# Optimization experiments

Hardware: AMD Instinct MI355X
Metric: run time of the kernel (lower is better)

The kernel has to match this reference:

```python
import jax, jax.numpy as jnp
import numpy as np

ALPHA = 10.0
DELTA = 0.0005
N = 16777216  # array_length


def setup_inputs() -> dict:
    key = jax.random.key(0)
    k1, k2 = jax.random.split(key)
    # learned parameter: in the original module this is initialized to linspace(0,1,N);
    # we use uniform [0,1] so the piecewise-linear search path is non-degenerate.
    indices = jax.random.uniform(k1, (N,), dtype=jnp.float32)
    array = jax.random.normal(k2, (N,), dtype=jnp.float32)
    return {"indices": indices, "array": array}


def reference(indices, array):
    # clamp learned knot positions to [0, 1]
    clamped = jnp.clip(indices, 0.0, 1.0)
    # piecewise-linear function f with x-knots = clamped, y-values = array.
    # jnp.interp requires ascending knots, so sort (x, y) pairs by x.
    order = jnp.argsort(clamped)
    xs = clamped[order]
    ys = array[order]
    # vectorized version of the per-index loop:
    #   left_item = f(clamped[i-1] + delta), this_item = f(clamped[i] - delta)
    q_left = clamped[:-1] + DELTA   # [N-1]
    q_this = clamped[1:] - DELTA    # [N-1]
    f_left = jnp.interp(q_left, xs, ys)
    f_this = jnp.interp(q_this, xs, ys)
    gap = jnp.maximum(f_left - f_this, 0.0)
    return ALPHA * jnp.sum(gap)
```

## Files before the change

### kernel.cpp

```cpp
#include <hip/hip_runtime.h>
#include <stdint.h>

#define ALPHA_C 10.0f
#define DELTA_C 0.0005f

typedef unsigned long long u64;
typedef unsigned u32;
typedef unsigned short u16;

#define KB2   (1u << 22)
#define NREG  8192
#define FPR   512
#define CAP   4096
#define Q38MAX ((1ULL << 38) - 1)

#define OLDKB (1u << 22)
#define SCAN_BLOCKS 1024
#define SCAN_TPB 256
#define SCAN_PER_THREAD 16

__device__ __forceinline__ float clamp01(float x) {
    return fminf(fmaxf(x, 0.0f), 1.0f);
}
__device__ __forceinline__ u64 q38_of(float x) {
    double d = (double)clamp01(x) * 274877906944.0;
    u64 q = (u64)d;
    return q > Q38MAX ? Q38MAX : q;
}
__device__ __forceinline__ u16 f2bf(float f) {
    u32 b = __float_as_uint(f);
    return (u16)((b + 0x8000u) >> 16);
}
__device__ __forceinline__ float bf2f(u32 h) {
    return __uint_as_float(h << 16);
}


__global__ void __launch_bounds__(256) k_hist(const float* __restrict__ ind,
                                              u32* __restrict__ cnt8k, int n) {
    __shared__ u32 lh[NREG];
    for (int k = threadIdx.x; k < (int)NREG; k += 256) lh[k] = 0;
    __syncthreads();
    int stride = gridDim.x * blockDim.x;
    for (int i = blockIdx.x * blockDim.x + threadIdx.x; i < n; i += stride)
        atomicAdd(&lh[(u32)(q38_of(ind[i]) >> 25)], 1u);
    __syncthreads();
    for (int k = threadIdx.x; k < (int)NREG; k += 256) {
        u32 v = lh[k];
        if (v) atomicAdd(&cnt8k[k], v);
    }
}

__global__ void __launch_bounds__(1024) k_scan8k(u32* __restrict__ cnt8k) {
    __shared__ u32 lds[1024];
    int tid = threadIdx.x;
    int base = tid * 8;
    u32 v[8]; u32 tot = 0;
#pragma unroll
    for (int k = 0; k < 8; ++k) { v[k] = cnt8k[base + k]; tot += v[k]; }
    lds[tid] = tot;
    __syncthreads();
    u32 x = tot;
    for (int s = 1; s < 1024; s <<= 1) {
        u32 y = (tid >= s) ? lds[tid - s] : 0u;
        __syncthreads();
        x += y; lds[tid] = x;
        __syncthreads();
    }
    u32 run = x - tot;
#pragma unroll
    for (int k = 0; k < 8; ++k) { u32 c = v[k]; cnt8k[base + k] = run; run += c; }
}

__global__ void k_coarse(const float* __restrict__ ind, const float* __restrict__ arr,
                         u32* __restrict__ cnt8k,
                         u32* __restrict__ recx, u64* __restrict__ reciy, int n) {
    int i = blockIdx.x * blockDim.x + threadIdx.x;
    if (i < n) {
        float x = ind[i];
        u32 r = (u32)(q38_of(x) >> 25);
        u32 e = atomicAdd(&cnt8k[r], 1u);
        recx[e] = __float_as_uint(x);
        reciy[e] = ((u64)(u32)i << 16) | (u64)f2bf(arr[i]);
    }
}

__global__ void __launch_bounds__(512) k_fine(const u32* __restrict__ cnt8k,
                                              u16* __restrict__ foff16,
                                              const u32* __restrict__ recx,
                                              u64* __restrict__ reciy_fdata) {
    __shared__ u32 sx[CAP];
    __shared__ u64 siy[CAP];
    __shared__ u32 incl[FPR];
    __shared__ u32 lexcl[FPR];
    __shared__ u32 lcnt[FPR];
    int r = blockIdx.x;
    u32 s = (r == 0) ? 0u : cnt8k[r - 1];
    u32 e = cnt8k[r];
    u32 cnt = e - s; if (cnt > CAP) cnt = CAP;
    for (u32 j = threadIdx.x; j < cnt; j += 512) { sx[j] = recx[s + j]; siy[j] = reciy_fdata[s + j]; }
    incl[threadIdx.x] = 0;
    lcnt[threadIdx.x] = 0;
    __syncthreads();
    for (u32 j = threadIdx.x; j < cnt; j += 512) {
        u32 lb = (u32)((q38_of(__uint_as_float(sx[j])) >> 16) & (FPR - 1));
        atomicAdd(&incl[lb], 1u);
    }
    __syncthreads();
    u32 myc = incl[threadIdx.x];
    u32 x = myc;
    for (int st = 1; st < FPR; st <<= 1) {
        u32 y = (threadIdx.x >= (u32)st) ? incl[threadIdx.x - st] : 0u;
        __syncthreads();
        x += y; incl[threadIdx.x] = x;
        __syncthreads();
    }
    lexcl[threadIdx.x] = x - myc;
    foff16[r * FPR + threadIdx.x] = (u16)x;
    __syncthreads();
    for (u32 j = threadIdx.x; j < cnt; j += 512) {
        u64 q = q38_of(__uint_as_float(sx[j]));
        u32 lb = (u32)((q >> 16) & (FPR - 1));
        u32 p = s + lexcl[lb] + atomicAdd(&lcnt[lb], 1u);
        u64 iy = siy[j];
        reciy_fdata[p] = ((q & 0xFFFFULL) << 40) | ((iy & 0xFFFFULL) << 24) | (iy >> 16);
    }
}

__device__ __forceinline__ void bucket_range(u32 b, const u32* __restrict__ cnt8k,
                                             const u16* __restrict__ foff16,
                                             u32* s, u32* e) {
    u32 r = b >> 9;
    u32 rbase = r ? cnt8k[r - 1] : 0u;
    u32 lb = b & (FPR - 1);
    *s = rbase + (lb ? (u32)foff16[b - 1] : 0u);
    *e = rbase + (u32)foff16[b];
}

__device__ float feval_q(u64 qq, const u32* __restrict__ cnt8k,
                         const u16* __restrict__ foff16, const u64* __restrict__ fdata) {
    u32 qb = (u32)(qq >> 16);
    u32 ql = (u32)(qq & 0xFFFFu);
    u32 s, e;
    bucket_range(qb, cnt8k, foff16, &s, &e);
    long long loK = -1;
    u64 hiK = ~0ULL;
    float loY = 0.0f, hiY = 0.0f;
    for (u32 p = s; p < e; ++p) {
        u64 d = fdata[p];
        u32 xlo = (u32)(d >> 40);
        u64 key = ((((u64)qb << 16) | xlo) << 24) | (d & 0xFFFFFFULL);
        float y = bf2f((u32)(d >> 24) & 0xFFFFu);
        if (xlo <= ql) { if ((long long)key >= loK) { loK = (long long)key; loY = y; } }
        else           { if (key < hiK)             { hiK = key;            hiY = y; } }
    }
    if (loK < 0) {
        u32 bl = qb;
        while (bl > 0) {
            --bl;
            u32 s2, e2;
            bucket_range(bl, cnt8k, foff16, &s2, &e2);
            if (e2 > s2) {
                for (u32 p = s2; p < e2; ++p) {
                    u64 d = fdata[p];
                    u64 key = ((((u64)bl << 16) | (d >> 40)) << 24) | (d & 0xFFFFFFULL);
                    if ((long long)key >= loK) { loK = (long long)key; loY = bf2f((u32)(d >> 24) & 0xFFFFu); }
                }
                break;
            }
        }
    }
    if (hiK == ~0ULL) {
        u32 br = qb;
        while (br < KB2 - 1) {
            ++br;
            u32 s2, e2;
            bucket_range(br, cnt8k, foff16, &s2, &e2);
            if (e2 > s2) {
                for (u32 p = s2; p < e2; ++p) {
                    u64 d = fdata[p];
                    u64 key = ((((u64)br << 16) | (d >> 40)) << 24) | (d & 0xFFFFFFULL);
                    if (key < hiK) { hiK = key; hiY = bf2f((u32)(d >> 24) & 0xFFFFu); }
                }
                break;
            }
        }
    }
    if (loK < 0) return hiY;
    if (hiK == ~0ULL) return loY;
    u64 loQ = (u64)loK >> 24;
    u64 hiQ = hiK >> 24;
    if (hiQ == loQ) return loY;
    float dq = (float)(qq - loQ);
    float dd = (float)(hiQ - loQ);
    return loY + (dq / dd) * (hiY - loY);
}

__global__ void __launch_bounds__(512) k_eval(const u32* __restrict__ cnt8k,
        const u16* __restrict__ foff16, const u64* __restrict__ fdata,
        u32* __restrict__ oval) {
    __shared__ u32 fend[FPR];
    int r = blockIdx.x;
    u32 s = r ? cnt8k[r - 1] : 0u;
    u32 e = cnt8k[r];
    fend[threadIdx.x] = s + (u32)foff16[r * FPR + threadIdx.x];
    __syncthreads();
    for (u32 t = s + threadIdx.x; t < e; t += 512) {
        u64 d = fdata[t];
        u32 lo = 0;
#pragma unroll
        for (u32 st = 256; st; st >>= 1) if (t >= fend[lo + st - 1]) lo += st;
        u64 xq = (((u64)((u32)r * FPR + lo)) << 16) | (d >> 40);
        u32 i = (u32)(d & 0xFFFFFFu);
        float x = (float)((double)xq * 3.63797880709171295e-12);
        float qpf = x + DELTA_C;
        float qmf = x - DELTA_C;
        u64 qp = q38_of(qpf);
        u64 qm = q38_of(qmf);
        float fp = feval_q(qp, cnt8k, foff16, fdata);
        float fm = feval_q(qm, cnt8k, foff16, fdata);
        oval[i] = ((u32)f2bf(fp) << 16) | (u32)f2bf(fm);
    }
}

__global__ void __launch_bounds__(256) k_pair2(const u32* __restrict__ oval,
                                               float* __restrict__ out, int n) {
    int stride = gridDim.x * blockDim.x;
    float sum = 0.0f;
    for (int j = blockIdx.x * blockDim.x + threadIdx.x; j < n - 1; j += stride) {
        u32 a = oval[j], b = oval[j + 1];
        sum += fmaxf(bf2f(a >> 16) - bf2f(b & 0xFFFFu), 0.0f);
    }
    float w = sum;
    for (int s = 32; s > 0; s >>= 1) w += __shfl_down(w, s, 64);
    __shared__ float wsum[4];
    if ((threadIdx.x & 63) == 0) wsum[threadIdx.x >> 6] = w;
    __syncthreads();
    if (threadIdx.x == 0)
        atomicAdd(out, ALPHA_C * (wsum[0] + wsum[1] + wsum[2] + wsum[3]));
}


__device__ __forceinline__ int bucket_of(float x) {
    int b = (int)(x * (float)OLDKB);
    b = b < 0 ? 0 : b;
    b = b > (int)OLDKB - 1 ? (int)OLDKB - 1 : b;
    return b;
}

__global__ void scan1(u32* __restrict__ off, u32* __restrict__ bsums) {
    __shared__ u32 lds[SCAN_TPB];
    int base = blockIdx.x * (SCAN_TPB * SCAN_PER_THREAD) + threadIdx.x * SCAN_PER_THREAD;
    u32 v[SCAN_PER_THREAD];
    u32 tot = 0;
#pragma unroll
    for (int k = 0; k < SCAN_PER_THREAD; ++k) { v[k] = off[base + k]; tot += v[k]; }
    lds[threadIdx.x] = tot;
    __syncthreads();
    u32 x = tot;
    for (int s = 1; s < SCAN_TPB; s <<= 1) {
        u32 y = (threadIdx.x >= (u32)s) ? lds[threadIdx.x - s] : 0u;
        __syncthreads();
        x += y; lds[threadIdx.x] = x;
        __syncthreads();
    }
    if (threadIdx.x == SCAN_TPB - 1) bsums[blockIdx.x] = x;
    u32 run = x - tot;
#pragma unroll
    for (int k = 0; k < SCAN_PER_THREAD; ++k) { u32 c = v[k]; off[base + k] = run; run += c; }
}

__global__ void scan2(u32* __restrict__ bsums) {
    __shared__ u32 lds[SCAN_BLOCKS];
    int tid = threadIdx.x;
    u32 v = bsums[tid];
    lds[tid] = v;
    __syncthreads();
    u32 x = v;
    for (int s = 1; s < SCAN_BLOCKS; s <<= 1) {
        u32 y = (tid >= s) ? lds[tid - s] : 0u;
        __syncthreads();
        x += y; lds[tid] = x;
        __syncthreads();
    }
    bsums[tid] = x - v;
}

__global__ void scan3(u32* __restrict__ off, const u32* __restrict__ bsums) {
    int base = blockIdx.x * (SCAN_TPB * SCAN_PER_THREAD);
    u32 add = bsums[blockIdx.x];
#pragma unroll
    for (int k = 0; k < SCAN_PER_THREAD; ++k)
        off[base + k * SCAN_TPB + threadIdx.x] += add;
}

__global__ void hist_kernel(const float* __restrict__ ind, u32* __restrict__ off, int n) {
    int i = blockIdx.x * blockDim.x + threadIdx.x;
    if (i < n) atomicAdd(&off[bucket_of(clamp01(ind[i]))], 1u);
}

__global__ void scatter_kernel(const float* __restrict__ ind, const float* __restrict__ arr,
                               u32* __restrict__ off, float2* __restrict__ buck, int n) {
    int i = blockIdx.x * blockDim.x + threadIdx.x;
    if (i < n) {
        float x = clamp01(ind[i]);
        u32 p = atomicAdd(&off[bucket_of(x)], 1u);
        buck[p] = make_float2(x, arr[i]);
    }
}

__device__ float feval(float q, const u32* __restrict__ off, const float2* __restrict__ buck) {
    int b = bucket_of(q);
    u32 s = (b == 0) ? 0u : off[b - 1];
    u32 e = off[b];
    float loX = -1e30f, loY = 0.0f, hiX = 1e30f, hiY = 0.0f;
    for (u32 u = s; u < e; ++u) {
        float2 p = buck[u];
        if (p.x <= q) { if (p.x >= loX) { loX = p.x; loY = p.y; } }
        else          { if (p.x <  hiX) { hiX = p.x; hiY = p.y; } }
    }
    if (loX == -1e30f) {
        int bl = b;
        while (bl > 0) {
            --bl;
            u32 s2 = (bl == 0) ? 0u : off[bl - 1];
            u32 e2 = off[bl];
            if (e2 > s2) {
                for (u32 u = s2; u < e2; ++u) {
                    float2 p = buck[u];
                    if (p.x >= loX) { loX = p.x; loY = p.y; }
                }
                break;
            }
        }
    }
    if (hiX == 1e30f) {
        int br = b;
        while (br < (int)OLDKB - 1) {
            ++br;
            u32 s2 = off[br - 1];
            u32 e2 = off[br];
            if (e2 > s2) {
                for (u32 u = s2; u < e2; ++u) {
                    float2 p = buck[u];
                    if (p.x < hiX) { hiX = p.x; hiY = p.y; }
                }
                break;
            }
        }
    }
    if (loX == -1e30f) return hiY;
    if (hiX ==  1e30f) return loY;
    return loY + (q - loX) * (hiY - loY) / (hiX - loX);
}

__global__ void query_kernel(const float* __restrict__ ind, const u32* __restrict__ off,
                             const float2* __restrict__ buck, float* __restrict__ out, int nterm) {
    int j = blockIdx.x * blockDim.x + threadIdx.x;
    float term = 0.0f;
    if (j < nterm) {
        float c0 = clamp01(ind[j]);
        float c1 = clamp01(ind[j + 1]);
        float fa = feval(c0 + DELTA_C, off, buck);
        float fb = feval(c1 - DELTA_C, off, buck);
        term = fmaxf(fa - fb, 0.0f);
    }
    float w = term;
    for (int s = 32; s > 0; s >>= 1) w += __shfl_down(w, s, 64);
    __shared__ float wsum[4];
    if ((threadIdx.x & 63) == 0) wsum[threadIdx.x >> 6] = w;
    __syncthreads();
    if (threadIdx.x == 0) atomicAdd(out, ALPHA_C * (wsum[0] + wsum[1] + wsum[2] + wsum[3]));
}


extern "C" void kernel_launch(void* const* d_in, const int* in_sizes, int n_in,
                              void* d_out, int out_size, void* d_ws, size_t ws_size,
                              hipStream_t stream) {
    const float* ind = (const float*)d_in[0];
    const float* arr = (const float*)d_in[1];
    float* out = (float*)d_out;
    int n = in_sizes[0];

    const int tpb = 256;
    int nblk = (n + tpb - 1) / tpb;
    uint8_t* w = (uint8_t*)d_ws;

    const size_t FOFF_SZ = (size_t)KB2 * 2;
    const size_t AUX = (size_t)1 << 20;
    size_t SZ8 = (size_t)n * 8, SZ4 = (size_t)n * 4;
    size_t base = FOFF_SZ + AUX;
    size_t need = base + SZ8 + SZ4;

    if (n <= (1 << 24) && ws_size >= need) {
        u16* foff16 = (u16*)w;
        u32* cnt8k  = (u32*)(w + FOFF_SZ);
        u64* reciy  = (u64*)(w + base);
        u32* recx   = (u32*)(w + base + SZ8);
        u32* oval   = (u32*)recx;

        hipMemsetAsync(cnt8k, 0, NREG * 4, stream);
        hipMemsetAsync(out, 0, sizeof(float) * (size_t)out_size, stream);

        k_hist<<<512, 256, 0, stream>>>(ind, cnt8k, n);
        k_scan8k<<<1, 1024, 0, stream>>>(cnt8k);
        k_coarse<<<nblk, tpb, 0, stream>>>(ind, arr, cnt8k, recx, reciy, n);
        k_fine<<<NREG, 512, 0, stream>>>(cnt8k, foff16, recx, reciy);
        k_eval<<<NREG, 512, 0, stream>>>(cnt8k, foff16, reciy, oval);
        k_pair2<<<2048, 256, 0, stream>>>(oval, out, n);
    } else {
        const size_t FO = (size_t)OLDKB * 4;
        u32* off = (u32*)w;
        u32* bsums = (u32*)(w + FO);
        float2* buck = (float2*)(w + FO + 4096);

        hipMemsetAsync(off, 0, FO, stream);
        hipMemsetAsync(out, 0, sizeof(float) * (size_t)out_size, stream);

        hist_kernel<<<nblk, tpb, 0, stream>>>(ind, off, n);
        scan1<<<SCAN_BLOCKS, SCAN_TPB, 0, stream>>>(off, bsums);
        scan2<<<1, SCAN_BLOCKS, 0, stream>>>(bsums);
        scan3<<<SCAN_BLOCKS, SCAN_TPB, 0, stream>>>(off, bsums);
        scatter_kernel<<<nblk, tpb, 0, stream>>>(ind, arr, off, buck, n);
        int nterm = n - 1;
        query_kernel<<<(nterm + tpb - 1) / tpb, tpb, 0, stream>>>(ind, off, buck, out, nterm);
    }
}
```

Before: 1.610 ms.

## Replace per-element coarse scatter with block-aggregated bucket scatter and fused fine sort

Replaces the coarse scatter, which did one global atomic per element, with a chunked kernel. Each block builds a shared-memory histogram over 4096 buckets, reserves ranges with one global atomic per bucket, then scatters packed 64-bit records. The fine sort now handles two coarse regions per block, reads the array values there rather than in the coarse pass, and writes the final packed records in place. cnt8k semantics shift from inclusive to exclusive offsets, which costs an extra prep kernel and a capacity limit (CAPB) that can truncate crowded buckets.

```diff
diff --git a/kernel.cpp b/kernel.cpp
--- a/kernel.cpp
+++ b/kernel.cpp
@@ -11,7 +11,11 @@
 #define KB2   (1u << 22)
 #define NREG  8192
 #define FPR   512
-#define CAP   4096
+#define NBK   4096
+#define RPB   2
+#define FPB   1024
+#define CAPB  4800
+#define ACHUNK 32768
 #define Q38MAX ((1ULL << 38) - 1)
 
 #define OLDKB (1u << 22)
@@ -72,58 +76,95 @@
     for (int k = 0; k < 8; ++k) { u32 c = v[k]; cnt8k[base + k] = run; run += c; }
 }
 
-__global__ void k_coarse(const float* __restrict__ ind, const float* __restrict__ arr,
-                         u32* __restrict__ cnt8k,
-                         u32* __restrict__ recx, u64* __restrict__ reciy, int n) {
-    int i = blockIdx.x * blockDim.x + threadIdx.x;
-    if (i < n) {
-        float x = ind[i];
-        u32 r = (u32)(q38_of(x) >> 25);
-        u32 e = atomicAdd(&cnt8k[r], 1u);
-        recx[e] = __float_as_uint(x);
-        reciy[e] = ((u64)(u32)i << 16) | (u64)f2bf(arr[i]);
-    }
-}
-
-__global__ void __launch_bounds__(512) k_fine(const u32* __restrict__ cnt8k,
-                                              u16* __restrict__ foff16,
-                                              const u32* __restrict__ recx,
-                                              u64* __restrict__ reciy_fdata) {
-    __shared__ u32 sx[CAP];
-    __shared__ u64 siy[CAP];
-    __shared__ u32 incl[FPR];
-    __shared__ u32 lexcl[FPR];
-    __shared__ u32 lcnt[FPR];
-    int r = blockIdx.x;
-    u32 s = (r == 0) ? 0u : cnt8k[r - 1];
-    u32 e = cnt8k[r];
-    u32 cnt = e - s; if (cnt > CAP) cnt = CAP;
-    for (u32 j = threadIdx.x; j < cnt; j += 512) { sx[j] = recx[s + j]; siy[j] = reciy_fdata[s + j]; }
-    incl[threadIdx.x] = 0;
-    lcnt[threadIdx.x] = 0;
-    __syncthreads();
-    for (u32 j = threadIdx.x; j < cnt; j += 512) {
-        u32 lb = (u32)((q38_of(__uint_as_float(sx[j])) >> 16) & (FPR - 1));
-        atomicAdd(&incl[lb], 1u);
-    }
-    __syncthreads();
-    u32 myc = incl[threadIdx.x];
-    u32 x = myc;
-    for (int st = 1; st < FPR; st <<= 1) {
-        u32 y = (threadIdx.x >= (u32)st) ? incl[threadIdx.x - st] : 0u;
-        __syncthreads();
-        x += y; incl[threadIdx.x] = x;
-        __syncthreads();
-    }
-    lexcl[threadIdx.x] = x - myc;
-    foff16[r * FPR + threadIdx.x] = (u16)x;
-    __syncthreads();
-    for (u32 j = threadIdx.x; j < cnt; j += 512) {
-        u64 q = q38_of(__uint_as_float(sx[j]));
-        u32 lb = (u32)((q >> 16) & (FPR - 1));
-        u32 p = s + lexcl[lb] + atomicAdd(&lcnt[lb], 1u);
-        u64 iy = siy[j];
-        reciy_fdata[p] = ((q & 0xFFFFULL) << 40) | ((iy & 0xFFFFULL) << 24) | (iy >> 16);
+__global__ void k_prep(const u32* __restrict__ cnt8k, u32* __restrict__ bcur) {
+    int b = blockIdx.x * 256 + threadIdx.x;
+    if (b < (int)NBK) bcur[b] = cnt8k[b * RPB];
+}
+
+__global__ void __launch_bounds__(256) k_bucket(const float* __restrict__ ind,
+                                                u32* __restrict__ bcur,
+                                                u64* __restrict__ rec, int n) {
+    __shared__ u32 hist[NBK];
+    __shared__ u32 base[NBK];
+    int cbase = blockIdx.x * ACHUNK;
+    for (u32 k = threadIdx.x; k < (u32)NBK; k += 256) hist[k] = 0;
+    __syncthreads();
+    for (int k = threadIdx.x; k < ACHUNK; k += 256) {
+        int i = cbase + k;
+        if (i >= n) break;
+        u32 bk = (u32)(q38_of(ind[i]) >> 26);
+        atomicAdd(&hist[bk], 1u);
+    }
+    __syncthreads();
+    for (u32 k = threadIdx.x; k < (u32)NBK; k += 256) {
+        u32 h = hist[k];
+        base[k] = h ? atomicAdd(&bcur[k], h) : 0u;
+    }
+    __syncthreads();
+    for (int k = threadIdx.x; k < ACHUNK; k += 256) {
+        int i = cbase + k;
+        if (i >= n) break;
+        u64 q = q38_of(ind[i]);
+        u32 bk = (u32)(q >> 26);
+        u32 d = atomicAdd(&base[bk], 1u);
+        rec[d] = (q << 24) | (u64)(u32)i;
+    }
+}
+
+__global__ void __launch_bounds__(256) k_group_fine(const u32* __restrict__ cnt8k,
+                                                    const float* __restrict__ arr,
+                                                    u16* __restrict__ foff16,
+                                                    u64* __restrict__ rec, int n) {
+    __shared__ u64 srec[CAPB];
+    __shared__ u32 sc[FPB];
+    __shared__ u32 lad[256];
+    int b = blockIdx.x;
+    u32 S = cnt8k[b * RPB];
+    u32 E = (b * RPB + RPB < (int)NREG) ? cnt8k[b * RPB + RPB] : (u32)n;
+    u32 cnt = E - S; if (cnt > CAPB) cnt = CAPB;
+    for (u32 j = threadIdx.x; j < cnt; j += 256) srec[j] = rec[S + j];
+    for (u32 f = threadIdx.x; f < (u32)FPB; f += 256) sc[f] = 0;
+    __syncthreads();
+    for (u32 j = threadIdx.x; j < cnt; j += 256) {
+        u32 fb = (u32)(srec[j] >> 40) & (FPB - 1);
+        atomicAdd(&sc[fb], 1u);
+    }
+    __syncthreads();
+    u32 c0 = sc[threadIdx.x * 4 + 0], c1 = sc[threadIdx.x * 4 + 1];
+    u32 c2 = sc[threadIdx.x * 4 + 2], c3 = sc[threadIdx.x * 4 + 3];
+    u32 tsum = c0 + c1 + c2 + c3;
+    lad[threadIdx.x] = tsum;
+    __syncthreads();
+    u32 x = tsum;
+    for (int st = 1; st < 256; st <<= 1) {
+        u32 y = (threadIdx.x >= (u32)st) ? lad[threadIdx.x - st] : 0u;
+        __syncthreads();
+        x += y; lad[threadIdx.x] = x;
+        __syncthreads();
+    }
+    u32 ex = x - tsum;
+    u32 e0 = ex, e1 = ex + c0, e2 = ex + c0 + c1, e3 = ex + c0 + c1 + c2;
+    sc[threadIdx.x * 4 + 0] = e0; sc[threadIdx.x * 4 + 1] = e1;
+    sc[threadIdx.x * 4 + 2] = e2; sc[threadIdx.x * 4 + 3] = e3;
+    __syncthreads();
+    {
+        u32 fb0 = threadIdx.x * 4;
+        u32 rs0 = sc[fb0 & ~511u];
+        u32 gb  = (u32)b * FPB + fb0;
+        foff16[gb + 0] = (u16)(e0 + c0 - rs0);
+        foff16[gb + 1] = (u16)(e1 + c1 - rs0);
+        foff16[gb + 2] = (u16)(e2 + c2 - rs0);
+        foff16[gb + 3] = (u16)(e3 + c3 - rs0);
+    }
+    __syncthreads();
+    for (u32 j = threadIdx.x; j < cnt; j += 256) {
+        u64 v = srec[j];
+        u32 fb  = (u32)(v >> 40) & (FPB - 1);
+        u32 i   = (u32)(v & 0xFFFFFFu);
+        u32 xlo = (u32)(v >> 24) & 0xFFFFu;
+        u32 ybf = f2bf(arr[i]);
+        u32 pos = atomicAdd(&sc[fb], 1u);
+        rec[S + pos] = ((u64)xlo << 40) | ((u64)ybf << 24) | (u64)i;
     }
 }
 
@@ -131,7 +172,7 @@
                                              const u16* __restrict__ foff16,
                                              u32* s, u32* e) {
     u32 r = b >> 9;
-    u32 rbase = r ? cnt8k[r - 1] : 0u;
+    u32 rbase = cnt8k[r];
     u32 lb = b & (FPR - 1);
     *s = rbase + (lb ? (u32)foff16[b - 1] : 0u);
     *e = rbase + (u32)foff16[b];
@@ -198,11 +239,11 @@
 
 __global__ void __launch_bounds__(512) k_eval(const u32* __restrict__ cnt8k,
         const u16* __restrict__ foff16, const u64* __restrict__ fdata,
-        u32* __restrict__ oval) {
+        u32* __restrict__ oval, int n) {
     __shared__ u32 fend[FPR];
     int r = blockIdx.x;
-    u32 s = r ? cnt8k[r - 1] : 0u;
-    u32 e = cnt8k[r];
+    u32 s = cnt8k[r];
+    u32 e = (r + 1 < (int)NREG) ? cnt8k[r + 1] : (u32)n;
     fend[threadIdx.x] = s + (u32)foff16[r * FPR + threadIdx.x];
     __syncthreads();
     for (u32 t = s + threadIdx.x; t < e; t += 512) {
@@ -395,18 +436,20 @@
     if (n <= (1 << 24) && ws_size >= need) {
         u16* foff16 = (u16*)w;
         u32* cnt8k  = (u32*)(w + FOFF_SZ);
-        u64* reciy  = (u64*)(w + base);
-        u32* recx   = (u32*)(w + base + SZ8);
-        u32* oval   = (u32*)recx;
+        u32* bcur   = (u32*)(w + FOFF_SZ + 32768);
+        u64* rec    = (u64*)(w + base);
+        u32* oval   = (u32*)(w + base + SZ8);
 
         hipMemsetAsync(cnt8k, 0, NREG * 4, stream);
         hipMemsetAsync(out, 0, sizeof(float) * (size_t)out_size, stream);
 
+        int abks = (n + ACHUNK - 1) / ACHUNK;
         k_hist<<<512, 256, 0, stream>>>(ind, cnt8k, n);
         k_scan8k<<<1, 1024, 0, stream>>>(cnt8k);
-        k_coarse<<<nblk, tpb, 0, stream>>>(ind, arr, cnt8k, recx, reciy, n);
-        k_fine<<<NREG, 512, 0, stream>>>(cnt8k, foff16, recx, reciy);
-        k_eval<<<NREG, 512, 0, stream>>>(cnt8k, foff16, reciy, oval);
+        k_prep<<<(NBK + 255) / 256, 256, 0, stream>>>(cnt8k, bcur);
+        k_bucket<<<abks, 256, 0, stream>>>(ind, bcur, rec, n);
+        k_group_fine<<<NBK, 256, 0, stream>>>(cnt8k, arr, foff16, rec, n);
+        k_eval<<<NREG, 512, 0, stream>>>(cnt8k, foff16, rec, oval, n);
         k_pair2<<<2048, 256, 0, stream>>>(oval, out, n);
     } else {
         const size_t FO = (size_t)OLDKB * 4;
```

After: 1.774 ms. 1.1x slower.

## Replace per-element global atomic scatter with block-local histogram and bulk reservation

Applied to the files above, without the earlier changes.

The coarse bucketing pass no longer does one global atomicAdd per element. Each block of 256 threads handles a 65536-element chunk: it builds a shared-memory histogram of bucket ids, reserves space per bucket with a single global atomic, then scatters using shared atomics. A separate cursor array copied from the scanned offsets keeps the end-offset semantics that later kernels expect. This cuts global atomic contention, but it reads the inputs twice, reduces parallelism to only 256 blocks, and uses 32KB of LDS per block.

```diff
diff --git a/kernel.cpp b/kernel.cpp
--- a/kernel.cpp
+++ b/kernel.cpp
@@ -12,6 +12,7 @@
 #define NREG  8192
 #define FPR   512
 #define CAP   4096
+#define ACHUNK 65536
 #define Q38MAX ((1ULL << 38) - 1)
 
 #define OLDKB (1u << 22)
@@ -72,14 +73,37 @@
     for (int k = 0; k < 8; ++k) { u32 c = v[k]; cnt8k[base + k] = run; run += c; }
 }
 
-__global__ void k_coarse(const float* __restrict__ ind, const float* __restrict__ arr,
-                         u32* __restrict__ cnt8k,
-                         u32* __restrict__ recx, u64* __restrict__ reciy, int n) {
-    int i = blockIdx.x * blockDim.x + threadIdx.x;
-    if (i < n) {
+__global__ void k_prep8k(const u32* __restrict__ cnt8k, u32* __restrict__ bcur) {
+    int r = blockIdx.x * 256 + threadIdx.x;
+    if (r < (int)NREG) bcur[r] = cnt8k[r];
+}
+
+__global__ void __launch_bounds__(256) k_bucket12(const float* __restrict__ ind,
+                                                  const float* __restrict__ arr,
+                                                  u32* __restrict__ bcur,
+                                                  u32* __restrict__ recx,
+                                                  u64* __restrict__ reciy, int n) {
+    __shared__ u32 hist[NREG];
+    int cbase = blockIdx.x * ACHUNK;
+    for (u32 k = threadIdx.x; k < (u32)NREG; k += 256) hist[k] = 0;
+    __syncthreads();
+    for (int k = threadIdx.x; k < ACHUNK; k += 256) {
+        int i = cbase + k;
+        if (i >= n) break;
+        atomicAdd(&hist[(u32)(q38_of(ind[i]) >> 25)], 1u);
+    }
+    __syncthreads();
+    for (u32 k = threadIdx.x; k < (u32)NREG; k += 256) {
+        u32 h = hist[k];
+        hist[k] = h ? atomicAdd(&bcur[k], h) : 0u;
+    }
+    __syncthreads();
+    for (int k = threadIdx.x; k < ACHUNK; k += 256) {
+        int i = cbase + k;
+        if (i >= n) break;
         float x = ind[i];
         u32 r = (u32)(q38_of(x) >> 25);
-        u32 e = atomicAdd(&cnt8k[r], 1u);
+        u32 e = atomicAdd(&hist[r], 1u);
         recx[e] = __float_as_uint(x);
         reciy[e] = ((u64)(u32)i << 16) | (u64)f2bf(arr[i]);
     }
@@ -395,6 +419,7 @@
     if (n <= (1 << 24) && ws_size >= need) {
         u16* foff16 = (u16*)w;
         u32* cnt8k  = (u32*)(w + FOFF_SZ);
+        u32* bcur   = (u32*)(w + FOFF_SZ + 32768);
         u64* reciy  = (u64*)(w + base);
         u32* recx   = (u32*)(w + base + SZ8);
         u32* oval   = (u32*)recx;
@@ -402,11 +427,13 @@
         hipMemsetAsync(cnt8k, 0, NREG * 4, stream);
         hipMemsetAsync(out, 0, sizeof(float) * (size_t)out_size, stream);
 
+        int abks = (n + ACHUNK - 1) / ACHUNK;
         k_hist<<<512, 256, 0, stream>>>(ind, cnt8k, n);
         k_scan8k<<<1, 1024, 0, stream>>>(cnt8k);
-        k_coarse<<<nblk, tpb, 0, stream>>>(ind, arr, cnt8k, recx, reciy, n);
-        k_fine<<<NREG, 512, 0, stream>>>(cnt8k, foff16, recx, reciy);
-        k_eval<<<NREG, 512, 0, stream>>>(cnt8k, foff16, reciy, oval);
+        k_prep8k<<<(NREG + 255) / 256, 256, 0, stream>>>(cnt8k, bcur);
+        k_bucket12<<<abks, 256, 0, stream>>>(ind, arr, bcur, recx, reciy, n);
+        k_fine<<<NREG, 512, 0, stream>>>(bcur, foff16, recx, reciy);
+        k_eval<<<NREG, 512, 0, stream>>>(bcur, foff16, reciy, oval);
         k_pair2<<<2048, 256, 0, stream>>>(oval, out, n);
     } else {
         const size_t FO = (size_t)OLDKB * 4;
```

Result: slower. 1.831 ms (+13.7%).
